# Kernel optimization log

Measured on AMD Instinct MI355X. Metric: run time of the kernel, lower is better.

Reference implementation:

```python
import jax, jax.numpy as jnp
import numpy as np

K_MAX_X = 16
K_MAX_T = 16


def _k_actual(N, k_max):
    # low-mode indices [0..k_max] ++ [N-k_max..N-1], mapped to signed frequencies
    idx = np.concatenate([np.arange(k_max + 1), np.arange(N - k_max, N)]).astype(np.float32)
    return np.where(idx <= (N - 1) // 2, idx, idx - N)


def _phase(N, k_max, sign):
    # separable 1D truncated DFT factor: exp(sign*2*pi*i*k*n/N)/sqrt(N), shape [modes, N]
    k = _k_actual(N, k_max)
    n = np.arange(N, dtype=np.float32)
    ang = sign * 2.0 * np.pi * k[:, None] * n[None, :] / N
    return jnp.asarray((np.exp(1j * ang) / np.sqrt(N)).astype(np.complex64))


def setup_inputs() -> dict:
    key = jax.random.key(0)
    k1, k2, k3 = jax.random.split(key, 3)
    B, C_in, C_out, H, W = 16, 64, 64, 128, 128
    modes = 2 * K_MAX_X + 1  # 33
    scale = 1.0 / (C_in * C_out)
    x = jax.random.normal(k1, (B, C_in, H, W), dtype=jnp.float32)
    wr = scale * jax.random.uniform(k2, (C_in, C_out, modes, modes), dtype=jnp.float32)
    wi = scale * jax.random.uniform(k3, (C_in, C_out, modes, modes), dtype=jnp.float32)
    return {"x": x, "weights_real": wr, "weights_imag": wi}


def reference(x, weights_real, weights_imag):
    B, C, H, W = x.shape
    Px_f = _phase(H, K_MAX_X, -1.0)  # [mx, H]
    Pt_f = _phase(W, K_MAX_T, -1.0)  # [mt, W]
    Px_i = _phase(H, K_MAX_X, +1.0)
    Pt_i = _phase(W, K_MAX_T, +1.0)
    xc = x.astype(jnp.complex64)
    # truncated 2D DFT (separable): X[b,c,i,j]
    X = jnp.einsum('bcnm,in,jm->bcij', xc, Px_f, Pt_f)
    R = (weights_real + 1j * weights_imag).astype(jnp.complex64)
    out_kept = jnp.einsum('bcij,coij->boij', X, R)
    # truncated inverse DFT back to grid
    out = jnp.einsum('boij,in,jm->bonm', out_kept, Px_i, Pt_i)
    return jnp.real(out)
```

## Files before the change

### kernel.cpp

```cpp
#include <hip/hip_runtime.h>


#define NB   16
#define NC   64
#define NO   64
#define NH   128
#define NW   128
#define NM   33
#define WMODE (NM*NM)
#define MPAD  1092
#define XPM   1104
#define MG    69
#define NIMG 1024
#define NTOT (64*64*WMODE)

typedef __attribute__((ext_vector_type(8))) short s8v;
typedef __attribute__((ext_vector_type(4))) float f4v;

__device__ inline unsigned short f2bf(float f) {
  union { float f; unsigned u; } v; v.f = f;
  unsigned r = (v.u + 0x7FFFu + ((v.u >> 16) & 1u)) >> 16;
  return (unsigned short)r;
}

__device__ inline float bflo(unsigned u) {
  union { unsigned u; float f; } cv; cv.u = u << 16; return cv.f;
}
__device__ inline float bfhi(unsigned u) {
  union { unsigned u; float f; } cv; cv.u = u & 0xFFFF0000u; return cv.f;
}

__device__ inline s8v pack8(float4 a, float4 b) {
  s8v r;
  r[0] = (short)f2bf(a.x); r[1] = (short)f2bf(a.y);
  r[2] = (short)f2bf(a.z); r[3] = (short)f2bf(a.w);
  r[4] = (short)f2bf(b.x); r[5] = (short)f2bf(b.y);
  r[6] = (short)f2bf(b.z); r[7] = (short)f2bf(b.w);
  return r;
}

__device__ inline uint2 pack4(f4v a) {
  uint2 p;
  p.x = (unsigned)f2bf(a[0]) | ((unsigned)f2bf(a[1]) << 16);
  p.y = (unsigned)f2bf(a[2]) | ((unsigned)f2bf(a[3]) << 16);
  return p;
}

__device__ inline unsigned short phase_bf(int f, int x) {
  if (f >= 66) return 0;
  int g = (f < 33) ? f : f - 33;
  int fr = (g <= 16) ? g : g + 95;
  int ph = (fr * x) & 127;
  float ang = (float)ph * 0.04908738521234052f;
  float v = ((f < 33) ? cosf(ang) : sinf(ang)) * 0.08838834764831845f;
  return f2bf(v);
}

__global__ __launch_bounds__(256) void spc_tables(short* __restrict__ T1,
                                                  short* __restrict__ T2,
                                                  short* __restrict__ T3,
                                                  short* __restrict__ T4) {
  int tid = blockIdx.x * 256 + threadIdx.x;
  if (tid >= 49152) return;
  int f, x; short* dst;
  if (tid < 10240) {
    int e = tid & 7, l = (tid >> 3) & 63, q = tid >> 9;
    int ks = q / 5, jt = q - 5 * ks;
    f = jt * 16 + (l & 15); x = ks * 32 + (l >> 4) * 8 + e; dst = T1 + tid;
  } else if (tid < 20480) {
    int u = tid - 10240;
    int e = u & 7, l = (u >> 3) & 63, q = u >> 9;
    int it = q >> 2, ks = q & 3;
    f = it * 16 + (l & 15); x = ks * 32 + (l >> 4) * 8 + e; dst = T2 + u;
  } else if (tid < 36864) {
    int u = tid - 20480;
    int e = u & 7, l = (u >> 3) & 63, q = u >> 9;
    int cs = q >> 4, ks = (q >> 3) & 1, mt = q & 7;
    int j = ks * 32 + (l >> 4) * 8 + e;
    f = (j < 33) ? cs * 33 + j : 66;
    x = mt * 16 + (l & 15); dst = T3 + u;
  } else {
    int u = tid - 36864;
    int e = u & 7, l = (u >> 3) & 63, q = u >> 9;
    int nt = q / 3, ks = q - 3 * nt;
    int i2 = ks * 32 + (l >> 4) * 8 + e;
    if (i2 < 48) f = (i2 < 33) ? i2 : 66;
    else         f = (i2 - 48 < 33) ? 33 + (i2 - 48) : 66;
    x = nt * 16 + (l & 15); dst = T4 + u;
  }
  *dst = (short)phase_bf(f, x);
}

__global__ __launch_bounds__(256) void spc_wpack(const float* __restrict__ wr,
                                                 const float* __restrict__ wi,
                                                 unsigned* __restrict__ Wpk) {
  const int t = threadIdx.x;
  const size_t base = (size_t)blockIdx.x * 4096;
#pragma unroll 1
  for (int p = 0; p < 4; ++p) {
    const size_t L = base + (size_t)p * 1024 + (size_t)t * 4;
    if (L + 4 <= (size_t)NTOT) {
      float4 a = *reinterpret_cast<const float4*>(wr + L);
      float4 b = *reinterpret_cast<const float4*>(wi + L);
      float ae[4] = {a.x, a.y, a.z, a.w};
      float be[4] = {b.x, b.y, b.z, b.w};
#pragma unroll
      for (int e = 0; e < 4; ++e) {
        unsigned Li = (unsigned)L + e;
        unsigned co = Li / (unsigned)WMODE;
        unsigned m  = Li - co * (unsigned)WMODE;
        unsigned c = co >> 6, o = co & 63u;
        size_t D = ((((size_t)(o >> 1) * MG + (m >> 4)) * 64 + c) * 2 + (o & 1)) * 16 + (m & 15);
        Wpk[D] = (unsigned)f2bf(ae[e]) | ((unsigned)f2bf(be[e]) << 16);
      }
    } else {
#pragma unroll
      for (int e = 0; e < 4; ++e) {
        size_t Li = L + e;
        if (Li < (size_t)NTOT) {
          unsigned Lu = (unsigned)Li;
          unsigned co = Lu / (unsigned)WMODE;
          unsigned m  = Lu - co * (unsigned)WMODE;
          unsigned c = co >> 6, o = co & 63u;
          size_t D = ((((size_t)(o >> 1) * MG + (m >> 4)) * 64 + c) * 2 + (o & 1)) * 16 + (m & 15);
          Wpk[D] = (unsigned)f2bf(wr[Li]) | ((unsigned)f2bf(wi[Li]) << 16);
        }
      }
    }
  }
}

__global__ __launch_bounds__(256) void spc_fwd_mfma(const float* __restrict__ x,
                                                    const s8v* __restrict__ T1,
                                                    const s8v* __restrict__ T2,
                                                    unsigned* __restrict__ X2u) {
  __shared__ short Wt[80 * 128];
  __shared__ float Gs[80 * 84];
  const int t = threadIdx.x;
  const int l = t & 63;
  const int w = t >> 6;
  const int lr = l & 15;
  const int lg = l >> 4;
  const int img = blockIdx.x;
  const float* xp = x + (size_t)img * (NH * NW);

  for (int nn = 0; nn < 2; ++nn) {
    const int nt = 2 * w + nn;
    const float* xrow = xp + (nt * 16 + lr) * NW + lg * 8;
    s8v a[4];
#pragma unroll
    for (int ks = 0; ks < 4; ++ks) {
      float4 f0 = *reinterpret_cast<const float4*>(xrow + ks * 32);
      float4 f1 = *reinterpret_cast<const float4*>(xrow + ks * 32 + 4);
      a[ks] = pack8(f0, f1);
    }
#pragma unroll
    for (int jt = 0; jt < 5; ++jt) {
      f4v acc = {0.f, 0.f, 0.f, 0.f};
#pragma unroll
      for (int ks = 0; ks < 4; ++ks) {
        s8v b = T1[(ks * 5 + jt) * 64 + l];
        acc = __builtin_amdgcn_mfma_f32_16x16x32_bf16(a[ks], b, acc, 0, 0, 0);
      }
      int j = jt * 16 + lr;
      int g = ((nt * 16 + lg * 4) >> 2) ^ ((j & 7) << 2);
      *reinterpret_cast<uint2*>(&Wt[j * 128 + g * 4]) = pack4(acc);
    }
  }
  __syncthreads();

  for (int tix = w; tix < 25; tix += 4) {
    int it = tix / 5, j2 = tix - 5 * it;
    int jrow = j2 * 16 + lr;
    f4v acc = {0.f, 0.f, 0.f, 0.f};
#pragma unroll
    for (int ks = 0; ks < 4; ++ks) {
      s8v afr = T2[(it * 4 + ks) * 64 + l];
      int g = (ks * 8 + lg * 2) ^ ((jrow & 7) << 2);
      s8v b = *reinterpret_cast<const s8v*>(&Wt[jrow * 128 + g * 4]);
      acc = __builtin_amdgcn_mfma_f32_16x16x32_bf16(afr, b, acc, 0, 0, 0);
    }
    int gi = it * 16 + lg * 4;
#pragma unroll
    for (int r = 0; r < 4; ++r) Gs[(gi + r) * 84 + jrow] = acc[r];
  }
  __syncthreads();

  unsigned* X2p = X2u + (size_t)img * WMODE;
  for (int idx = t; idx < WMODE; idx += 256) {
    int i = idx / 33, j = idx - 33 * i;
    float g11 = Gs[i * 84 + j];
    float g22 = Gs[(i + 33) * 84 + (j + 33)];
    float g12 = Gs[i * 84 + (j + 33)];
    float g21 = Gs[(i + 33) * 84 + j];
    X2p[idx] = (unsigned)f2bf(g11 - g22) | ((unsigned)f2bf(-(g12 + g21)) << 16);
  }
}

__global__ __launch_bounds__(256) void spc_xrepack(const unsigned* __restrict__ X2u,
                                                   unsigned* __restrict__ Xp) {
  __shared__ unsigned Ls[32 * 65];
  const int t = threadIdx.x;
  const int l = t & 63;
  const int w = t >> 6;
  const int m0 = blockIdx.x * 64;
  const int c0 = blockIdx.y * 2;

  {
    unsigned vv[8];
    const int m = m0 + l;
#pragma unroll
    for (int rr = 0; rr < 8; ++rr) {
      int r = w * 8 + rr;
      int b = r & 15, cl = r >> 4;
      vv[rr] = (m < WMODE) ? X2u[(size_t)(b * 64 + c0 + cl) * WMODE + m] : 0u;
    }
#pragma unroll
    for (int rr = 0; rr < 8; ++rr)
      Ls[(w * 8 + rr) * 65 + l] = vv[rr];
  }
  __syncthreads();
  for (int p = 0; p < 8; ++p) {
    int m_l = p * 8 + w * 2 + (l >> 5);
    int m = m0 + m_l;
    if (m >= XPM) continue;
    int cl = (l >> 4) & 1, b = l & 15;
    unsigned v = Ls[(cl * 16 + b) * 65 + m_l];
    Xp[((size_t)m * 64 + c0 + cl) * 16 + b] = v;
  }
}

__global__ __launch_bounds__(512) void spc_vmix(const unsigned* __restrict__ Wpk,
                                                const unsigned* __restrict__ Xp,
                                                short* __restrict__ Kbf) {
  __shared__ unsigned Xl[16 * 1028];
  __shared__ unsigned Wl[2048];
  __shared__ unsigned short Ols[1024];
  const int t = threadIdx.x;
  const int l = t & 63;
  const int w = t >> 6;
  const int opair = blockIdx.x;
  const int mg = blockIdx.y;
  const int m0 = mg * 16;

  {
    const uint4* src = reinterpret_cast<const uint4*>(Xp + (size_t)m0 * 1024);
#pragma unroll
    for (int p = 0; p < 8; ++p) {
      int idx = p * 512 + t;
      int row = idx >> 8, col = idx & 255;
      *reinterpret_cast<uint4*>(&Xl[row * 1028 + col * 4]) = src[idx];
    }
  }
  if (t < 512) {
    const uint4* src = reinterpret_cast<const uint4*>(
        Wpk + ((size_t)opair * MG + mg) * 2048);
    *reinterpret_cast<uint4*>(&Wl[t * 4]) = src[t];
  }
  __syncthreads();

  const int bg = w >> 1, oo = w & 1;
  const int m_l = l >> 2, bl = l & 3;
  const int xbase = m_l * 1028 + bg * 4 + bl;
  const int wbase = oo * 16 + m_l;

  float aR = 0.f, aI = 0.f;
#pragma unroll 4
  for (int c = 0; c < 64; ++c) {
    unsigned xv = Xl[xbase + c * 16];
    unsigned wv = Wl[wbase + c * 32];
    float xr = bflo(xv), xi = bfhi(xv);
    float wre = bflo(wv), wim = bfhi(wv);
    aR = fmaf(xr, wre, fmaf(-xi, wim, aR));
    aI = fmaf(xr, wim, fmaf( xi, wre, aI));
  }

  const int b = bg * 4 + bl;
  Ols[((oo * 16 + b) * 2 + 0) * 16 + m_l] = f2bf(aR);
  Ols[((oo * 16 + b) * 2 + 1) * 16 + m_l] = f2bf(aI);
  __syncthreads();

  if (t < 256) {
    const int pair = t >> 2, q = t & 3;
    if (!(mg == 68 && q > 0)) {
      const int oo2 = pair >> 5, b2 = (pair >> 1) & 15, ri = pair & 1;
      const size_t img = (size_t)b2 * 64 + opair * 2 + oo2;
      uint2 v = *reinterpret_cast<const uint2*>(&Ols[pair * 16 + q * 4]);
      *reinterpret_cast<uint2*>(Kbf + img * (2 * MPAD) + (size_t)ri * MPAD + m0 + q * 4) = v;
    }
  }
}

__global__ __launch_bounds__(256) void spc_inv_mfma(const short* __restrict__ Kbf,
                                                    const s8v* __restrict__ T3,
                                                    const s8v* __restrict__ T4,
                                                    float* __restrict__ out) {
  __shared__ short Kls2[2 * MPAD];
  __shared__ short Vt[128 * 128];
  const int t = threadIdx.x;
  const int l = t & 63;
  const int w = t >> 6;
  const int lr = l & 15;
  const int lg = l >> 4;
  const int img = blockIdx.x;

  {
    const uint4* src = reinterpret_cast<const uint4*>(Kbf + (size_t)img * (2 * MPAD));
    uint4* dstl = reinterpret_cast<uint4*>(Kls2);
    for (int idx = t; idx < 273; idx += 256) dstl[idx] = src[idx];
  }
  __syncthreads();

  s8v fr[2][3][2];
#pragma unroll
  for (int ri2 = 0; ri2 < 2; ++ri2)
#pragma unroll
    for (int it = 0; it < 3; ++it)
#pragma unroll
      for (int ks = 0; ks < 2; ++ks) {
        const int i = it * 16 + lr;
#pragma unroll
        for (int e = 0; e < 8; ++e) {
          const int j = ks * 32 + lg * 8 + e;
          unsigned short v = (i < 33 && j < 33)
              ? (unsigned short)Kls2[ri2 * MPAD + i * 33 + j] : (unsigned short)0;
          fr[ri2][it][ks][e] = (short)v;
        }
      }

  for (int mm = 0; mm < 2; ++mm) {
    const int mt = w * 2 + mm;
    const int m = mt * 16 + lr;
    s8v cw[2], sw[2], nsw[2];
#pragma unroll
    for (int ks = 0; ks < 2; ++ks) {
      cw[ks] = T3[((0 * 2 + ks) * 8 + mt) * 64 + l];
      sw[ks] = T3[((1 * 2 + ks) * 8 + mt) * 64 + l];
#pragma unroll
      for (int e = 0; e < 8; ++e)
        nsw[ks][e] = (short)(((unsigned short)sw[ks][e]) ^ 0x8000u);
    }
#pragma unroll
    for (int it = 0; it < 3; ++it) {
      f4v t1 = {0.f, 0.f, 0.f, 0.f}, t2 = {0.f, 0.f, 0.f, 0.f};
#pragma unroll
      for (int ks = 0; ks < 2; ++ks) {
        t1 = __builtin_amdgcn_mfma_f32_16x16x32_bf16(fr[0][it][ks], cw[ks],  t1, 0, 0, 0);
        t1 = __builtin_amdgcn_mfma_f32_16x16x32_bf16(fr[1][it][ks], nsw[ks], t1, 0, 0, 0);
        t2 = __builtin_amdgcn_mfma_f32_16x16x32_bf16(fr[1][it][ks], cw[ks],  t2, 0, 0, 0);
        t2 = __builtin_amdgcn_mfma_f32_16x16x32_bf16(fr[0][it][ks], sw[ks],  t2, 0, 0, 0);
      }
      const int base1 = it * 16 + lg * 4;
      const int g1 = (base1 >> 2) ^ ((m & 7) << 2);
      *reinterpret_cast<uint2*>(&Vt[m * 128 + g1 * 4]) = pack4(t1);
      f4v nt2v = {-t2[0], -t2[1], -t2[2], -t2[3]};
      const int g2 = ((48 + base1) >> 2) ^ ((m & 7) << 2);
      *reinterpret_cast<uint2*>(&Vt[m * 128 + g2 * 4]) = pack4(nt2v);
    }
  }
  __syncthreads();

  float* op = out + (size_t)img * (NH * NW);
  for (int nn = 0; nn < 2; ++nn) {
    const int nt = w * 2 + nn;
    s8v a[3];
#pragma unroll
    for (int ks = 0; ks < 3; ++ks) a[ks] = T4[(nt * 3 + ks) * 64 + l];
    for (int mt = 0; mt < 8; ++mt) {
      const int m = mt * 16 + lr;
      f4v acc = {0.f, 0.f, 0.f, 0.f};
#pragma unroll
      for (int ks = 0; ks < 3; ++ks) {
        const int g = (ks * 8 + lg * 2) ^ ((m & 7) << 2);
        s8v bb = *reinterpret_cast<const s8v*>(&Vt[m * 128 + g * 4]);
        acc = __builtin_amdgcn_mfma_f32_16x16x32_bf16(a[ks], bb, acc, 0, 0, 0);
      }
      const int n = nt * 16 + lg * 4;
#pragma unroll
      for (int r = 0; r < 4; ++r) op[(n + r) * NW + m] = acc[r];
    }
  }
}

extern "C" void kernel_launch(void* const* d_in, const int* in_sizes, int n_in,
                              void* d_out, int out_size, void* d_ws, size_t ws_size,
                              hipStream_t stream) {
  const float* x  = (const float*)d_in[0];
  const float* wr = (const float*)d_in[1];
  const float* wi = (const float*)d_in[2];
  float* out = (float*)d_out;

  char* ws = (char*)d_ws;
  short* T1 = (short*)(ws);
  short* T2 = (short*)(ws + 20480);
  short* T3 = (short*)(ws + 40960);
  short* T4 = (short*)(ws + 73728);
  unsigned* X2u = (unsigned*)(ws + 98304);
  short* Kbf = (short*)(ws + 4558848);
  unsigned* Xp = (unsigned*)(ws + 9031680);
  unsigned* Wpk = (unsigned*)(ws + 13553664);

  hipLaunchKernelGGL(spc_tables, dim3(192), dim3(256), 0, stream, T1, T2, T3, T4);
  hipLaunchKernelGGL(spc_wpack, dim3(1090), dim3(256), 0, stream, wr, wi, Wpk);
  hipLaunchKernelGGL(spc_fwd_mfma, dim3(NIMG), dim3(256), 0, stream,
                     x, (const s8v*)T1, (const s8v*)T2, X2u);
  hipLaunchKernelGGL(spc_xrepack, dim3(18, 32), dim3(256), 0, stream, X2u, Xp);
  hipLaunchKernelGGL(spc_vmix, dim3(32, MG), dim3(512), 0, stream,
                     Wpk, Xp, Kbf);
  hipLaunchKernelGGL(spc_inv_mfma, dim3(NIMG), dim3(256), 0, stream,
                     Kbf, (const s8v*)T3, (const s8v*)T4, out);
}
```

Before: 90.11 us.

## Register-block spectral channel mix over 2x2 batch/output tiles with mode-chunk grid

```diff
diff --git a/kernel.cpp b/kernel.cpp
--- a/kernel.cpp
+++ b/kernel.cpp
@@ -8,11 +8,11 @@
 #define NW   128
 #define NM   33
 #define WMODE (NM*NM)
-#define MPAD  1092
-#define XPM   1104
-#define MG    69
+#define MPAD  1096
+#define XPM   1096
+#define NMCH  137
 #define NIMG 1024
-#define NTOT (64*64*WMODE)
+#define WLS   515
 
 typedef __attribute__((ext_vector_type(8))) short s8v;
 typedef __attribute__((ext_vector_type(4))) float f4v;
@@ -93,41 +93,23 @@
 
 __global__ __launch_bounds__(256) void spc_wpack(const float* __restrict__ wr,
                                                  const float* __restrict__ wi,
-                                                 unsigned* __restrict__ Wpk) {
+                                                 unsigned* __restrict__ W2) {
   const int t = threadIdx.x;
-  const size_t base = (size_t)blockIdx.x * 4096;
-#pragma unroll 1
-  for (int p = 0; p < 4; ++p) {
-    const size_t L = base + (size_t)p * 1024 + (size_t)t * 4;
-    if (L + 4 <= (size_t)NTOT) {
-      float4 a = *reinterpret_cast<const float4*>(wr + L);
-      float4 b = *reinterpret_cast<const float4*>(wi + L);
-      float ae[4] = {a.x, a.y, a.z, a.w};
-      float be[4] = {b.x, b.y, b.z, b.w};
-#pragma unroll
-      for (int e = 0; e < 4; ++e) {
-        unsigned Li = (unsigned)L + e;
-        unsigned co = Li / (unsigned)WMODE;
-        unsigned m  = Li - co * (unsigned)WMODE;
-        unsigned c = co >> 6, o = co & 63u;
-        size_t D = ((((size_t)(o >> 1) * MG + (m >> 4)) * 64 + c) * 2 + (o & 1)) * 16 + (m & 15);
-        Wpk[D] = (unsigned)f2bf(ae[e]) | ((unsigned)f2bf(be[e]) << 16);
-      }
-    } else {
-#pragma unroll
-      for (int e = 0; e < 4; ++e) {
-        size_t Li = L + e;
-        if (Li < (size_t)NTOT) {
-          unsigned Lu = (unsigned)Li;
-          unsigned co = Lu / (unsigned)WMODE;
-          unsigned m  = Lu - co * (unsigned)WMODE;
-          unsigned c = co >> 6, o = co & 63u;
-          size_t D = ((((size_t)(o >> 1) * MG + (m >> 4)) * 64 + c) * 2 + (o & 1)) * 16 + (m & 15);
-          Wpk[D] = (unsigned)f2bf(wr[Li]) | ((unsigned)f2bf(wi[Li]) << 16);
-        }
-      }
-    }
-  }
+  const int l = t & 63;
+  const int w = t >> 6;
+  const int row = blockIdx.x * 4 + w;
+  const int c = row >> 6, o = row & 63;
+  const float* rp = wr + (size_t)row * WMODE;
+  const float* ip = wi + (size_t)row * WMODE;
+  unsigned* dst = W2 + (size_t)c * 512 + (size_t)o * 8;
+  for (int it = 0; it < 18; ++it) {
+    const int m = it * 64 + l;
+    if (m < WMODE) {
+      unsigned v = (unsigned)f2bf(rp[m]) | ((unsigned)f2bf(ip[m]) << 16);
+      dst[(size_t)(m >> 3) * 32768 + (m & 7)] = v;
+    }
+  }
+  if (l < 7) dst[(size_t)136 * 32768 + 1 + l] = 0u;
 }
 
 __global__ __launch_bounds__(256) void spc_fwd_mfma(const float* __restrict__ x,
@@ -230,64 +212,84 @@
   }
 }
 
-__global__ __launch_bounds__(512) void spc_vmix(const unsigned* __restrict__ Wpk,
+__global__ __launch_bounds__(512) void spc_vmix(const unsigned* __restrict__ W2,
                                                 const unsigned* __restrict__ Xp,
                                                 short* __restrict__ Kbf) {
-  __shared__ unsigned Xl[16 * 1028];
-  __shared__ unsigned Wl[2048];
-  __shared__ unsigned short Ols[1024];
+  __shared__ unsigned Xl[8 * 1024];
+  __shared__ unsigned Wl[16 * WLS];
+  __shared__ unsigned short Ols[512 * 8];
   const int t = threadIdx.x;
   const int l = t & 63;
-  const int w = t >> 6;
-  const int opair = blockIdx.x;
-  const int mg = blockIdx.y;
-  const int m0 = mg * 16;
+  const int mq = t >> 6;
+  const int bq = l & 7;
+  const int oq = (l >> 3) & 7;
+  const int mc8 = blockIdx.x;
+  const int oqd = blockIdx.y;
 
   {
-    const uint4* src = reinterpret_cast<const uint4*>(Xp + (size_t)m0 * 1024);
-#pragma unroll
-    for (int p = 0; p < 8; ++p) {
-      int idx = p * 512 + t;
-      int row = idx >> 8, col = idx & 255;
-      *reinterpret_cast<uint4*>(&Xl[row * 1028 + col * 4]) = src[idx];
-    }
-  }
-  if (t < 512) {
-    const uint4* src = reinterpret_cast<const uint4*>(
-        Wpk + ((size_t)opair * MG + mg) * 2048);
-    *reinterpret_cast<uint4*>(&Wl[t * 4]) = src[t];
-  }
-  __syncthreads();
-
-  const int bg = w >> 1, oo = w & 1;
-  const int m_l = l >> 2, bl = l & 3;
-  const int xbase = m_l * 1028 + bg * 4 + bl;
-  const int wbase = oo * 16 + m_l;
-
-  float aR = 0.f, aI = 0.f;
+    const uint4* src = reinterpret_cast<const uint4*>(Xp + (size_t)mc8 * 8192);
+    uint4* dst = reinterpret_cast<uint4*>(Xl);
+#pragma unroll
+    for (int p = 0; p < 4; ++p) dst[p * 512 + t] = src[p * 512 + t];
+  }
+  {
+    const uint4* srcW = reinterpret_cast<const uint4*>(W2);
+#pragma unroll
+    for (int p = 0; p < 4; ++p) {
+      const int idx = p * 512 + t;
+      const int c = idx >> 5, r = idx & 31;
+      uint4 v = srcW[(size_t)mc8 * 8192 + c * 128 + oqd * 32 + r];
+      const int o_loc = r >> 1, ml4 = (r & 1) * 4;
+      unsigned* d = &Wl[o_loc * WLS + c * 8 + ml4];
+      d[0] = v.x; d[1] = v.y; d[2] = v.z; d[3] = v.w;
+    }
+  }
+  __syncthreads();
+
+  float aR[2][2], aI[2][2];
+#pragma unroll
+  for (int bb = 0; bb < 2; ++bb)
+#pragma unroll
+    for (int oo = 0; oo < 2; ++oo) { aR[bb][oo] = 0.f; aI[bb][oo] = 0.f; }
+
+  const int xb = mq * 1024 + 2 * bq;
+  const int wb = (2 * oq) * WLS + mq;
 #pragma unroll 4
   for (int c = 0; c < 64; ++c) {
-    unsigned xv = Xl[xbase + c * 16];
-    unsigned wv = Wl[wbase + c * 32];
-    float xr = bflo(xv), xi = bfhi(xv);
-    float wre = bflo(wv), wim = bfhi(wv);
-    aR = fmaf(xr, wre, fmaf(-xi, wim, aR));
-    aI = fmaf(xr, wim, fmaf( xi, wre, aI));
-  }
-
-  const int b = bg * 4 + bl;
-  Ols[((oo * 16 + b) * 2 + 0) * 16 + m_l] = f2bf(aR);
-  Ols[((oo * 16 + b) * 2 + 1) * 16 + m_l] = f2bf(aI);
-  __syncthreads();
-
-  if (t < 256) {
-    const int pair = t >> 2, q = t & 3;
-    if (!(mg == 68 && q > 0)) {
-      const int oo2 = pair >> 5, b2 = (pair >> 1) & 15, ri = pair & 1;
-      const size_t img = (size_t)b2 * 64 + opair * 2 + oo2;
-      uint2 v = *reinterpret_cast<const uint2*>(&Ols[pair * 16 + q * 4]);
-      *reinterpret_cast<uint2*>(Kbf + img * (2 * MPAD) + (size_t)ri * MPAD + m0 + q * 4) = v;
-    }
+    const unsigned x0 = Xl[xb + c * 16 + 0];
+    const unsigned x1 = Xl[xb + c * 16 + 1];
+    const unsigned w0 = Wl[wb + c * 8];
+    const unsigned w1 = Wl[wb + WLS + c * 8];
+    const float xr0 = bflo(x0), xi0 = bfhi(x0);
+    const float xr1 = bflo(x1), xi1 = bfhi(x1);
+    const float wr0 = bflo(w0), wi0 = bfhi(w0);
+    const float wr1 = bflo(w1), wi1 = bfhi(w1);
+    aR[0][0] = fmaf(xr0, wr0, fmaf(-xi0, wi0, aR[0][0]));
+    aI[0][0] = fmaf(xr0, wi0, fmaf( xi0, wr0, aI[0][0]));
+    aR[0][1] = fmaf(xr0, wr1, fmaf(-xi0, wi1, aR[0][1]));
+    aI[0][1] = fmaf(xr0, wi1, fmaf( xi0, wr1, aI[0][1]));
+    aR[1][0] = fmaf(xr1, wr0, fmaf(-xi1, wi0, aR[1][0]));
+    aI[1][0] = fmaf(xr1, wi0, fmaf( xi1, wr0, aI[1][0]));
+    aR[1][1] = fmaf(xr1, wr1, fmaf(-xi1, wi1, aR[1][1]));
+    aI[1][1] = fmaf(xr1, wi1, fmaf( xi1, wr1, aI[1][1]));
+  }
+
+#pragma unroll
+  for (int bb = 0; bb < 2; ++bb)
+#pragma unroll
+    for (int oo = 0; oo < 2; ++oo) {
+      const int bo = (2 * bq + bb) * 16 + 2 * oq + oo;
+      Ols[(bo * 2 + 0) * 8 + mq] = f2bf(aR[bb][oo]);
+      Ols[(bo * 2 + 1) * 8 + mq] = f2bf(aI[bb][oo]);
+    }
+  __syncthreads();
+
+  {
+    const int ri = t & 1, bo = t >> 1;
+    const int b = bo >> 4, o_loc = bo & 15;
+    const size_t img = (size_t)b * 64 + oqd * 16 + o_loc;
+    uint4 v = *reinterpret_cast<const uint4*>(&Ols[t * 8]);
+    *reinterpret_cast<uint4*>(Kbf + img * (2 * MPAD) + (size_t)ri * MPAD + mc8 * 8) = v;
   }
 }
 
@@ -307,7 +309,7 @@
   {
     const uint4* src = reinterpret_cast<const uint4*>(Kbf + (size_t)img * (2 * MPAD));
     uint4* dstl = reinterpret_cast<uint4*>(Kls2);
-    for (int idx = t; idx < 273; idx += 256) dstl[idx] = src[idx];
+    for (int idx = t; idx < 274; idx += 256) dstl[idx] = src[idx];
   }
   __syncthreads();
 
@@ -397,16 +399,15 @@
   short* T4 = (short*)(ws + 73728);
   unsigned* X2u = (unsigned*)(ws + 98304);
   short* Kbf = (short*)(ws + 4558848);
-  unsigned* Xp = (unsigned*)(ws + 9031680);
-  unsigned* Wpk = (unsigned*)(ws + 13553664);
+  unsigned* Xp = (unsigned*)(ws + 9048064);
+  unsigned* W2 = (unsigned*)(ws + 13537280);
 
   hipLaunchKernelGGL(spc_tables, dim3(192), dim3(256), 0, stream, T1, T2, T3, T4);
-  hipLaunchKernelGGL(spc_wpack, dim3(1090), dim3(256), 0, stream, wr, wi, Wpk);
+  hipLaunchKernelGGL(spc_wpack, dim3(1024), dim3(256), 0, stream, wr, wi, W2);
   hipLaunchKernelGGL(spc_fwd_mfma, dim3(NIMG), dim3(256), 0, stream,
                      x, (const s8v*)T1, (const s8v*)T2, X2u);
   hipLaunchKernelGGL(spc_xrepack, dim3(18, 32), dim3(256), 0, stream, X2u, Xp);
-  hipLaunchKernelGGL(spc_vmix, dim3(32, MG), dim3(512), 0, stream,
-                     Wpk, Xp, Kbf);
+  hipLaunchKernelGGL(spc_vmix, dim3(NMCH, 4), dim3(512), 0, stream, W2, Xp, Kbf);
   hipLaunchKernelGGL(spc_inv_mfma, dim3(NIMG), dim3(256), 0, stream,
                      Kbf, (const s8v*)T3, (const s8v*)T4, out);
 }
```

New measurement: 82.99 us. 1.09x faster.
